# Optimization experiments

Measured on AMD Instinct MI355X. Metric: run time of the kernel, lower is better.

## Reference

```python
import jax, jax.numpy as jnp
import numpy as np
import math

D_MODEL = 512
NHEAD = 8
D_K = D_MODEL // NHEAD
WINDOW = 128
BATCH = 1
SEQ = 4096
NEG = -1e9  # matches torch masked_fill value


def setup_inputs() -> dict:
    key = jax.random.key(0)
    ks = jax.random.split(key, 9)
    s = 1.0 / math.sqrt(D_MODEL)
    return {
        "x": jax.random.normal(ks[0], (BATCH, SEQ, D_MODEL), dtype=jnp.float32),
        "wq": jax.random.uniform(ks[1], (D_MODEL, D_MODEL), jnp.float32, -s, s),
        "bq": jax.random.uniform(ks[2], (D_MODEL,), jnp.float32, -s, s),
        "wk": jax.random.uniform(ks[3], (D_MODEL, D_MODEL), jnp.float32, -s, s),
        "bk": jax.random.uniform(ks[4], (D_MODEL,), jnp.float32, -s, s),
        "wv": jax.random.uniform(ks[5], (D_MODEL, D_MODEL), jnp.float32, -s, s),
        "bv": jax.random.uniform(ks[6], (D_MODEL,), jnp.float32, -s, s),
        "wo": jax.random.uniform(ks[7], (D_MODEL, D_MODEL), jnp.float32, -s, s),
        "bo": jax.random.uniform(ks[8], (D_MODEL,), jnp.float32, -s, s),
    }


def reference(x, wq, bq, wk, bk, wv, bv, wo, bo):
    B, S, D = x.shape
    # projections -> (B, H, S, d_k)
    q = (x @ wq.T + bq).reshape(B, S, NHEAD, D_K).transpose(0, 2, 1, 3)
    k = (x @ wk.T + bk).reshape(B, S, NHEAD, D_K).transpose(0, 2, 1, 3)
    v = (x @ wv.T + bv).reshape(B, S, NHEAD, D_K).transpose(0, 2, 1, 3)
    # dense scores, band-masked (faithful to original: full S x S)
    scores = jnp.einsum('bhqd,bhkd->bhqk', q, k) / math.sqrt(D_K)
    idx = jnp.arange(S)
    band = jnp.abs(idx[:, None] - idx[None, :]) <= WINDOW  # (S, S)
    scores = jnp.where(band[None, None], scores, NEG)
    attn = jax.nn.softmax(scores, axis=-1)  # (B, H, S, S)
    ctx = jnp.einsum('bhqk,bhkd->bhqd', attn, v)
    ctx = ctx.transpose(0, 2, 1, 3).reshape(B, S, D)
    out = ctx @ wo.T + bo
    return out, attn
```

## Files before the change

kernel.cpp:

```cpp
#include <hip/hip_runtime.h>
#include <hip/hip_bf16.h>
#include <math.h>

#define S 4096
#define D 512
#define H 8
#define DK 64
#define WIN 128

typedef __attribute__((ext_vector_type(8))) short bf16x8;
typedef __attribute__((ext_vector_type(4))) float f32x4;

__device__ __forceinline__ unsigned short f2bf(float f) {
    __hip_bfloat16 h = __float2bfloat16(f);
    return *(unsigned short*)&h;
}

__global__ __launch_bounds__(256) void conv_bf16_kernel(
    const float* __restrict__ in, unsigned short* __restrict__ out, int n)
{
    const int i = (blockIdx.x * 256 + threadIdx.x) * 8;
    if (i >= n) return;
    float4 a = *(const float4*)&in[i];
    float4 b = *(const float4*)&in[i + 4];
    ushort4 o0 = {f2bf(a.x), f2bf(a.y), f2bf(a.z), f2bf(a.w)};
    ushort4 o1 = {f2bf(b.x), f2bf(b.y), f2bf(b.z), f2bf(b.w)};
    *(ushort4*)&out[i]     = o0;
    *(ushort4*)&out[i + 4] = o1;
}

__device__ __forceinline__ void mfma_gemm_body(
    const unsigned short* __restrict__ A,
    const float* __restrict__ W,
    const float* __restrict__ bias,
    float* __restrict__ C,
    unsigned short* __restrict__ CB)
{
    __shared__ unsigned short Bs[64][520];

    const int tid  = threadIdx.x;
    const int m0   = blockIdx.x * 128;
    const int n0   = blockIdx.y * 64;
    const int wv   = tid >> 6;
    const int lane = tid & 63;
    const int l16  = lane & 15;
    const int klo  = (lane >> 4) * 8;

    #pragma unroll
    for (int it = 0; it < 16; ++it) {
        const int c   = tid + it * 256;
        const int row = c >> 6;
        const int kc  = (c & 63) * 8;
        const float* src = &W[(size_t)(n0 + row) * 512 + kc];
        float4 a = *(const float4*)&src[0];
        float4 b = *(const float4*)&src[4];
        ushort4 o0 = {f2bf(a.x), f2bf(a.y), f2bf(a.z), f2bf(a.w)};
        ushort4 o1 = {f2bf(b.x), f2bf(b.y), f2bf(b.z), f2bf(b.w)};
        *(ushort4*)&Bs[row][kc]     = o0;
        *(ushort4*)&Bs[row][kc + 4] = o1;
    }
    __syncthreads();

    const unsigned short* arow0 = &A[(size_t)(m0 + wv * 32 + l16) * 512 + klo];
    const unsigned short* arow1 = arow0 + 16 * 512;

    f32x4 acc[2][4];
    #pragma unroll
    for (int r = 0; r < 2; ++r)
        #pragma unroll
        for (int nf = 0; nf < 4; ++nf)
            acc[r][nf] = (f32x4){0.f, 0.f, 0.f, 0.f};

    #pragma unroll 4
    for (int kb = 0; kb < 512; kb += 32) {
        bf16x8 a0 = *(const bf16x8*)&arow0[kb];
        bf16x8 a1 = *(const bf16x8*)&arow1[kb];
        #pragma unroll
        for (int nf = 0; nf < 4; ++nf) {
            bf16x8 b = *(const bf16x8*)&Bs[nf * 16 + l16][kb + klo];
            acc[0][nf] = __builtin_amdgcn_mfma_f32_16x16x32_bf16(a0, b, acc[0][nf], 0, 0, 0);
            acc[1][nf] = __builtin_amdgcn_mfma_f32_16x16x32_bf16(a1, b, acc[1][nf], 0, 0, 0);
        }
    }

    const int r0 = (lane >> 4) * 4;
    #pragma unroll
    for (int r = 0; r < 2; ++r) {
        #pragma unroll
        for (int nf = 0; nf < 4; ++nf) {
            const int col = n0 + nf * 16 + l16;
            const float bb = bias[col];
            #pragma unroll
            for (int vv = 0; vv < 4; ++vv) {
                const int row = m0 + wv * 32 + r * 16 + r0 + vv;
                const float val = acc[r][nf][vv] + bb;
                if (C)  C [(size_t)row * 512 + col] = val;
                if (CB) CB[(size_t)row * 512 + col] = f2bf(val);
            }
        }
    }
}

__global__ __launch_bounds__(256) void proj3_kernel(
    const unsigned short* __restrict__ xb,
    const float* __restrict__ wq, const float* __restrict__ bq,
    const float* __restrict__ wk, const float* __restrict__ bk,
    const float* __restrict__ wv, const float* __restrict__ bv,
    unsigned short* __restrict__ qb, unsigned short* __restrict__ kb,
    unsigned short* __restrict__ vb)
{
    const float* W; const float* b; unsigned short* CB;
    if (blockIdx.z == 0)      { W = wq; b = bq; CB = qb; }
    else if (blockIdx.z == 1) { W = wk; b = bk; CB = kb; }
    else                      { W = wv; b = bv; CB = vb; }
    mfma_gemm_body(xb, W, b, nullptr, CB);
}

__global__ __launch_bounds__(256) void outproj_kernel(
    const unsigned short* __restrict__ ctxb,
    const float* __restrict__ wo, const float* __restrict__ bo,
    float* __restrict__ out)
{
    mfma_gemm_body(ctxb, wo, bo, out, nullptr);
}

__global__ __launch_bounds__(256) void band_attn_kernel(
    const unsigned short* __restrict__ qb, const unsigned short* __restrict__ kb,
    const unsigned short* __restrict__ vb,
    float* __restrict__ attn, unsigned short* __restrict__ ctxb)
{
    __shared__ __align__(16) unsigned short Qs[16][72];
    __shared__ __align__(16) unsigned short KV[64][72];
    __shared__ float P[16][336];
    __shared__ float rinvs[16];

    const int tid = threadIdx.x;
    const int h  = blockIdx.y;
    const int q0 = blockIdx.x * 16;
    const int w0 = q0 - 128;

    const int wv   = tid >> 6;
    const int lane = tid & 63;
    const int l16  = lane & 15;
    const int klo  = (lane >> 4) * 8;
    const int r0   = (lane >> 4) * 4;

    {
        const int row = tid >> 4;
        const int db  = (tid & 15) * 4;
        *(ushort4*)&Qs[row][db] =
            *(const ushort4*)&qb[(size_t)(q0 + row) * 512 + h * 64 + db];
    }

    const int lr = tid >> 2;
    const int ld = (tid & 3) * 16;

    for (int ch = 0; ch < 5; ++ch) {
        const int c0 = w0 + ch * 64;
        if (c0 + 64 <= 0 || c0 >= S) continue;
        __syncthreads();
        {
            const int krow = min(max(c0 + lr, 0), S - 1);
            const unsigned short* src = &kb[(size_t)krow * 512 + h * 64 + ld];
            *(bf16x8*)&KV[lr][ld]     = *(const bf16x8*)&src[0];
            *(bf16x8*)&KV[lr][ld + 8] = *(const bf16x8*)&src[8];
        }
        __syncthreads();

        f32x4 acc = (f32x4){0.f, 0.f, 0.f, 0.f};
        #pragma unroll
        for (int kk = 0; kk < 64; kk += 32) {
            bf16x8 a = *(const bf16x8*)&Qs[l16][kk + klo];
            bf16x8 b = *(const bf16x8*)&KV[wv * 16 + l16][kk + klo];
            acc = __builtin_amdgcn_mfma_f32_16x16x32_bf16(a, b, acc, 0, 0, 0);
        }
        #pragma unroll
        for (int vv = 0; vv < 4; ++vv)
            P[r0 + vv][ch * 64 + wv * 16 + l16] = acc[vv] * 0.125f;
    }
    __syncthreads();

    {
        const int r   = tid >> 4;
        const int lx  = tid & 15;
        const int i   = q0 + r;
        const int lo = max(i - WIN, 0) - w0;
        const int hi = min(i + WIN, S - 1) - w0;

        float m = -1e30f;
        for (int c = lo + lx; c <= hi; c += 16) m = fmaxf(m, P[r][c]);
        m = fmaxf(m, __shfl_xor(m, 1));
        m = fmaxf(m, __shfl_xor(m, 2));
        m = fmaxf(m, __shfl_xor(m, 4));
        m = fmaxf(m, __shfl_xor(m, 8));

        float sum = 0.f;
        for (int c = lx; c < 320; c += 16) {
            float e = 0.f;
            if (c >= lo && c <= hi) {
                e = __expf(P[r][c] - m);
                sum += e;
            }
            P[r][c] = e;
        }
        sum += __shfl_xor(sum, 1);
        sum += __shfl_xor(sum, 2);
        sum += __shfl_xor(sum, 4);
        sum += __shfl_xor(sum, 8);
        if (lx == 0) rinvs[r] = 1.0f / sum;
    }

    f32x4 pacc = (f32x4){0.f, 0.f, 0.f, 0.f};
    for (int ch = 0; ch < 5; ++ch) {
        const int c0 = w0 + ch * 64;
        if (c0 + 64 <= 0 || c0 >= S) continue;
        __syncthreads();
        {
            const int vrow = min(max(c0 + lr, 0), S - 1);
            ushort4 v0 = *(const ushort4*)&vb[(size_t)vrow * 512 + h * 64 + ld];
            ushort4 v1 = *(const ushort4*)&vb[(size_t)vrow * 512 + h * 64 + ld + 4];
            ushort4 v2 = *(const ushort4*)&vb[(size_t)vrow * 512 + h * 64 + ld + 8];
            ushort4 v3 = *(const ushort4*)&vb[(size_t)vrow * 512 + h * 64 + ld + 12];
            KV[ld +  0][lr] = v0.x; KV[ld +  1][lr] = v0.y;
            KV[ld +  2][lr] = v0.z; KV[ld +  3][lr] = v0.w;
            KV[ld +  4][lr] = v1.x; KV[ld +  5][lr] = v1.y;
            KV[ld +  6][lr] = v1.z; KV[ld +  7][lr] = v1.w;
            KV[ld +  8][lr] = v2.x; KV[ld +  9][lr] = v2.y;
            KV[ld + 10][lr] = v2.z; KV[ld + 11][lr] = v2.w;
            KV[ld + 12][lr] = v3.x; KV[ld + 13][lr] = v3.y;
            KV[ld + 14][lr] = v3.z; KV[ld + 15][lr] = v3.w;
        }
        __syncthreads();

        #pragma unroll
        for (int kk = 0; kk < 64; kk += 32) {
            unsigned short abuf[8];
            #pragma unroll
            for (int e = 0; e < 8; ++e)
                abuf[e] = f2bf(P[l16][ch * 64 + kk + klo + e]);
            bf16x8 a = *(const bf16x8*)abuf;
            bf16x8 b = *(const bf16x8*)&KV[wv * 16 + l16][kk + klo];
            pacc = __builtin_amdgcn_mfma_f32_16x16x32_bf16(a, b, pacc, 0, 0, 0);
        }
    }

    #pragma unroll
    for (int vv = 0; vv < 4; ++vv) {
        const int row = q0 + r0 + vv;
        ctxb[(size_t)row * 512 + h * 64 + wv * 16 + l16] =
            f2bf(pacc[vv] * rinvs[r0 + vv]);
    }

    float* rowbase = attn + (size_t)h * S * S;
    #pragma unroll 1
    for (int r = 0; r < 16; ++r) {
        const int i = q0 + r;
        float* rowp = rowbase + (size_t)i * S;
        const int lo = max(i - WIN, 0) - w0;
        const int hi = min(i + WIN, S - 1) - w0;
        const float rv = rinvs[r];
        #pragma unroll
        for (int t = 0; t < 4; ++t) {
            const int c4 = (tid + t * 256) << 2;
            const int lc = c4 - w0;
            float4 o;
            if (lc >= lo && lc + 3 <= hi) {
                float4 p = *(const float4*)&P[r][lc];
                o.x = p.x * rv; o.y = p.y * rv; o.z = p.z * rv; o.w = p.w * rv;
            } else if (lc + 3 < lo || lc > hi) {
                o = make_float4(0.f, 0.f, 0.f, 0.f);
            } else {
                o.x = (lc + 0 >= lo && lc + 0 <= hi) ? P[r][lc + 0] * rv : 0.f;
                o.y = (lc + 1 >= lo && lc + 1 <= hi) ? P[r][lc + 1] * rv : 0.f;
                o.z = (lc + 2 >= lo && lc + 2 <= hi) ? P[r][lc + 2] * rv : 0.f;
                o.w = (lc + 3 >= lo && lc + 3 <= hi) ? P[r][lc + 3] * rv : 0.f;
            }
            *(float4*)&rowp[c4] = o;
        }
    }
}

extern "C" void kernel_launch(void* const* d_in, const int* in_sizes, int n_in,
                              void* d_out, int out_size, void* d_ws, size_t ws_size,
                              hipStream_t stream)
{
    (void)in_sizes; (void)n_in; (void)out_size; (void)ws_size;
    const float* x  = (const float*)d_in[0];
    const float* wq = (const float*)d_in[1];
    const float* bq = (const float*)d_in[2];
    const float* wk = (const float*)d_in[3];
    const float* bk = (const float*)d_in[4];
    const float* wv = (const float*)d_in[5];
    const float* bv = (const float*)d_in[6];
    const float* wo = (const float*)d_in[7];
    const float* bo = (const float*)d_in[8];

    float* out  = (float*)d_out;
    float* attn = out + (size_t)S * D;

    unsigned short* xb   = (unsigned short*)d_ws;
    unsigned short* qb   = xb   + (size_t)S * D;
    unsigned short* kb   = qb   + (size_t)S * D;
    unsigned short* vb   = kb   + (size_t)S * D;
    unsigned short* ctxb = vb   + (size_t)S * D;

    conv_bf16_kernel<<<(S * D) / (256 * 8), 256, 0, stream>>>(x, xb, S * D);
    proj3_kernel<<<dim3(32, 8, 3), 256, 0, stream>>>(xb, wq, bq, wk, bk, wv, bv, qb, kb, vb);
    band_attn_kernel<<<dim3(256, 8), 256, 0, stream>>>(qb, kb, vb, attn, ctxb);
    outproj_kernel<<<dim3(32, 8), 256, 0, stream>>>(ctxb, wo, bo, out);
}
```

Measured before the change: 153.3 us.

## Pre-convert weights to bf16, read B from global, warp-local KV staging, nontemporal attn stores

All weight matrices are converted to bf16 once in the conversion kernel, so the GEMM blocks no longer convert fp32 weights into shared memory and instead read bf16 B fragments straight from global memory. In the band attention kernel, each wave now stages only the K/V rows it consumes, and the block-wide barriers around each chunk are replaced by a local LDS wait. The large attn output is written with nontemporal stores to reduce cache pollution. The GEMM now relies on cache hits for B reuse rather than LDS, and the conversion kernel launches many idle blocks for the smaller weight tensors.

```diff
diff --git a/kernel.cpp b/kernel.cpp
--- a/kernel.cpp
+++ b/kernel.cpp
@@ -17,27 +17,38 @@
 }
 
 __global__ __launch_bounds__(256) void conv_bf16_kernel(
-    const float* __restrict__ in, unsigned short* __restrict__ out, int n)
-{
+    const float* __restrict__ x,
+    const float* __restrict__ wq, const float* __restrict__ wk,
+    const float* __restrict__ wv, const float* __restrict__ wo,
+    unsigned short* __restrict__ xb,
+    unsigned short* __restrict__ wqb, unsigned short* __restrict__ wkb,
+    unsigned short* __restrict__ wvb, unsigned short* __restrict__ wob)
+{
+    const float* src; unsigned short* dst; int n;
+    switch (blockIdx.y) {
+        case 0:  src = x;  dst = xb;  n = S * D; break;
+        case 1:  src = wq; dst = wqb; n = D * D; break;
+        case 2:  src = wk; dst = wkb; n = D * D; break;
+        case 3:  src = wv; dst = wvb; n = D * D; break;
+        default: src = wo; dst = wob; n = D * D; break;
+    }
     const int i = (blockIdx.x * 256 + threadIdx.x) * 8;
     if (i >= n) return;
-    float4 a = *(const float4*)&in[i];
-    float4 b = *(const float4*)&in[i + 4];
+    float4 a = *(const float4*)&src[i];
+    float4 b = *(const float4*)&src[i + 4];
     ushort4 o0 = {f2bf(a.x), f2bf(a.y), f2bf(a.z), f2bf(a.w)};
     ushort4 o1 = {f2bf(b.x), f2bf(b.y), f2bf(b.z), f2bf(b.w)};
-    *(ushort4*)&out[i]     = o0;
-    *(ushort4*)&out[i + 4] = o1;
+    *(ushort4*)&dst[i]     = o0;
+    *(ushort4*)&dst[i + 4] = o1;
 }
 
 __device__ __forceinline__ void mfma_gemm_body(
     const unsigned short* __restrict__ A,
-    const float* __restrict__ W,
+    const unsigned short* __restrict__ W16,
     const float* __restrict__ bias,
     float* __restrict__ C,
     unsigned short* __restrict__ CB)
 {
-    __shared__ unsigned short Bs[64][520];
-
     const int tid  = threadIdx.x;
     const int m0   = blockIdx.x * 128;
     const int n0   = blockIdx.y * 64;
@@ -46,23 +57,9 @@
     const int l16  = lane & 15;
     const int klo  = (lane >> 4) * 8;
 
-    #pragma unroll
-    for (int it = 0; it < 16; ++it) {
-        const int c   = tid + it * 256;
-        const int row = c >> 6;
-        const int kc  = (c & 63) * 8;
-        const float* src = &W[(size_t)(n0 + row) * 512 + kc];
-        float4 a = *(const float4*)&src[0];
-        float4 b = *(const float4*)&src[4];
-        ushort4 o0 = {f2bf(a.x), f2bf(a.y), f2bf(a.z), f2bf(a.w)};
-        ushort4 o1 = {f2bf(b.x), f2bf(b.y), f2bf(b.z), f2bf(b.w)};
-        *(ushort4*)&Bs[row][kc]     = o0;
-        *(ushort4*)&Bs[row][kc + 4] = o1;
-    }
-    __syncthreads();
-
     const unsigned short* arow0 = &A[(size_t)(m0 + wv * 32 + l16) * 512 + klo];
     const unsigned short* arow1 = arow0 + 16 * 512;
+    const unsigned short* brow  = &W16[(size_t)(n0 + l16) * 512 + klo];
 
     f32x4 acc[2][4];
     #pragma unroll
@@ -77,7 +74,7 @@
         bf16x8 a1 = *(const bf16x8*)&arow1[kb];
         #pragma unroll
         for (int nf = 0; nf < 4; ++nf) {
-            bf16x8 b = *(const bf16x8*)&Bs[nf * 16 + l16][kb + klo];
+            bf16x8 b = *(const bf16x8*)&brow[nf * 16 * 512 + kb];
             acc[0][nf] = __builtin_amdgcn_mfma_f32_16x16x32_bf16(a0, b, acc[0][nf], 0, 0, 0);
             acc[1][nf] = __builtin_amdgcn_mfma_f32_16x16x32_bf16(a1, b, acc[1][nf], 0, 0, 0);
         }
@@ -103,25 +100,25 @@
 
 __global__ __launch_bounds__(256) void proj3_kernel(
     const unsigned short* __restrict__ xb,
-    const float* __restrict__ wq, const float* __restrict__ bq,
-    const float* __restrict__ wk, const float* __restrict__ bk,
-    const float* __restrict__ wv, const float* __restrict__ bv,
+    const unsigned short* __restrict__ wqb, const float* __restrict__ bq,
+    const unsigned short* __restrict__ wkb, const float* __restrict__ bk,
+    const unsigned short* __restrict__ wvb, const float* __restrict__ bv,
     unsigned short* __restrict__ qb, unsigned short* __restrict__ kb,
     unsigned short* __restrict__ vb)
 {
-    const float* W; const float* b; unsigned short* CB;
-    if (blockIdx.z == 0)      { W = wq; b = bq; CB = qb; }
-    else if (blockIdx.z == 1) { W = wk; b = bk; CB = kb; }
-    else                      { W = wv; b = bv; CB = vb; }
+    const unsigned short* W; const float* b; unsigned short* CB;
+    if (blockIdx.z == 0)      { W = wqb; b = bq; CB = qb; }
+    else if (blockIdx.z == 1) { W = wkb; b = bk; CB = kb; }
+    else                      { W = wvb; b = bv; CB = vb; }
     mfma_gemm_body(xb, W, b, nullptr, CB);
 }
 
 __global__ __launch_bounds__(256) void outproj_kernel(
     const unsigned short* __restrict__ ctxb,
-    const float* __restrict__ wo, const float* __restrict__ bo,
+    const unsigned short* __restrict__ wob, const float* __restrict__ bo,
     float* __restrict__ out)
 {
-    mfma_gemm_body(ctxb, wo, bo, out, nullptr);
+    mfma_gemm_body(ctxb, wob, bo, out, nullptr);
 }
 
 __global__ __launch_bounds__(256) void band_attn_kernel(
@@ -151,21 +148,20 @@
         *(ushort4*)&Qs[row][db] =
             *(const ushort4*)&qb[(size_t)(q0 + row) * 512 + h * 64 + db];
     }
-
-    const int lr = tid >> 2;
-    const int ld = (tid & 3) * 16;
+    __syncthreads();
 
     for (int ch = 0; ch < 5; ++ch) {
         const int c0 = w0 + ch * 64;
         if (c0 + 64 <= 0 || c0 >= S) continue;
-        __syncthreads();
         {
-            const int krow = min(max(c0 + lr, 0), S - 1);
-            const unsigned short* src = &kb[(size_t)krow * 512 + h * 64 + ld];
-            *(bf16x8*)&KV[lr][ld]     = *(const bf16x8*)&src[0];
-            *(bf16x8*)&KV[lr][ld + 8] = *(const bf16x8*)&src[8];
-        }
-        __syncthreads();
+            const int kcol = wv * 16 + (lane & 15);
+            const int dd   = (lane >> 4) * 16;
+            const int krow = min(max(c0 + kcol, 0), S - 1);
+            const unsigned short* src = &kb[(size_t)krow * 512 + h * 64 + dd];
+            *(bf16x8*)&KV[kcol][dd]     = *(const bf16x8*)&src[0];
+            *(bf16x8*)&KV[kcol][dd + 8] = *(const bf16x8*)&src[8];
+        }
+        asm volatile("s_waitcnt lgkmcnt(0)" ::: "memory");
 
         f32x4 acc = (f32x4){0.f, 0.f, 0.f, 0.f};
         #pragma unroll
@@ -209,28 +205,30 @@
         sum += __shfl_xor(sum, 8);
         if (lx == 0) rinvs[r] = 1.0f / sum;
     }
+    __syncthreads();
 
     f32x4 pacc = (f32x4){0.f, 0.f, 0.f, 0.f};
     for (int ch = 0; ch < 5; ++ch) {
         const int c0 = w0 + ch * 64;
         if (c0 + 64 <= 0 || c0 >= S) continue;
-        __syncthreads();
         {
-            const int vrow = min(max(c0 + lr, 0), S - 1);
-            ushort4 v0 = *(const ushort4*)&vb[(size_t)vrow * 512 + h * 64 + ld];
-            ushort4 v1 = *(const ushort4*)&vb[(size_t)vrow * 512 + h * 64 + ld + 4];
-            ushort4 v2 = *(const ushort4*)&vb[(size_t)vrow * 512 + h * 64 + ld + 8];
-            ushort4 v3 = *(const ushort4*)&vb[(size_t)vrow * 512 + h * 64 + ld + 12];
-            KV[ld +  0][lr] = v0.x; KV[ld +  1][lr] = v0.y;
-            KV[ld +  2][lr] = v0.z; KV[ld +  3][lr] = v0.w;
-            KV[ld +  4][lr] = v1.x; KV[ld +  5][lr] = v1.y;
-            KV[ld +  6][lr] = v1.z; KV[ld +  7][lr] = v1.w;
-            KV[ld +  8][lr] = v2.x; KV[ld +  9][lr] = v2.y;
-            KV[ld + 10][lr] = v2.z; KV[ld + 11][lr] = v2.w;
-            KV[ld + 12][lr] = v3.x; KV[ld + 13][lr] = v3.y;
-            KV[ld + 14][lr] = v3.z; KV[ld + 15][lr] = v3.w;
-        }
-        __syncthreads();
+            const int col  = lane;
+            const int vrow = min(max(c0 + col, 0), S - 1);
+            const unsigned short* src = &vb[(size_t)vrow * 512 + h * 64 + wv * 16];
+            ushort4 v0 = *(const ushort4*)&src[0];
+            ushort4 v1 = *(const ushort4*)&src[4];
+            ushort4 v2 = *(const ushort4*)&src[8];
+            ushort4 v3 = *(const ushort4*)&src[12];
+            KV[wv * 16 +  0][col] = v0.x; KV[wv * 16 +  1][col] = v0.y;
+            KV[wv * 16 +  2][col] = v0.z; KV[wv * 16 +  3][col] = v0.w;
+            KV[wv * 16 +  4][col] = v1.x; KV[wv * 16 +  5][col] = v1.y;
+            KV[wv * 16 +  6][col] = v1.z; KV[wv * 16 +  7][col] = v1.w;
+            KV[wv * 16 +  8][col] = v2.x; KV[wv * 16 +  9][col] = v2.y;
+            KV[wv * 16 + 10][col] = v2.z; KV[wv * 16 + 11][col] = v2.w;
+            KV[wv * 16 + 12][col] = v3.x; KV[wv * 16 + 13][col] = v3.y;
+            KV[wv * 16 + 14][col] = v3.z; KV[wv * 16 + 15][col] = v3.w;
+        }
+        asm volatile("s_waitcnt lgkmcnt(0)" ::: "memory");
 
         #pragma unroll
         for (int kk = 0; kk < 64; kk += 32) {
@@ -263,19 +261,19 @@
         for (int t = 0; t < 4; ++t) {
             const int c4 = (tid + t * 256) << 2;
             const int lc = c4 - w0;
-            float4 o;
+            f32x4 o;
             if (lc >= lo && lc + 3 <= hi) {
-                float4 p = *(const float4*)&P[r][lc];
-                o.x = p.x * rv; o.y = p.y * rv; o.z = p.z * rv; o.w = p.w * rv;
+                f32x4 p = *(const f32x4*)&P[r][lc];
+                o = p * rv;
             } else if (lc + 3 < lo || lc > hi) {
-                o = make_float4(0.f, 0.f, 0.f, 0.f);
+                o = (f32x4){0.f, 0.f, 0.f, 0.f};
             } else {
-                o.x = (lc + 0 >= lo && lc + 0 <= hi) ? P[r][lc + 0] * rv : 0.f;
-                o.y = (lc + 1 >= lo && lc + 1 <= hi) ? P[r][lc + 1] * rv : 0.f;
-                o.z = (lc + 2 >= lo && lc + 2 <= hi) ? P[r][lc + 2] * rv : 0.f;
-                o.w = (lc + 3 >= lo && lc + 3 <= hi) ? P[r][lc + 3] * rv : 0.f;
+                o[0] = (lc + 0 >= lo && lc + 0 <= hi) ? P[r][lc + 0] * rv : 0.f;
+                o[1] = (lc + 1 >= lo && lc + 1 <= hi) ? P[r][lc + 1] * rv : 0.f;
+                o[2] = (lc + 2 >= lo && lc + 2 <= hi) ? P[r][lc + 2] * rv : 0.f;
+                o[3] = (lc + 3 >= lo && lc + 3 <= hi) ? P[r][lc + 3] * rv : 0.f;
             }
-            *(float4*)&rowp[c4] = o;
+            __builtin_nontemporal_store(o, (f32x4*)&rowp[c4]);
         }
     }
 }
@@ -303,9 +301,15 @@
     unsigned short* kb   = qb   + (size_t)S * D;
     unsigned short* vb   = kb   + (size_t)S * D;
     unsigned short* ctxb = vb   + (size_t)S * D;
-
-    conv_bf16_kernel<<<(S * D) / (256 * 8), 256, 0, stream>>>(x, xb, S * D);
-    proj3_kernel<<<dim3(32, 8, 3), 256, 0, stream>>>(xb, wq, bq, wk, bk, wv, bv, qb, kb, vb);
+    unsigned short* wqb  = ctxb + (size_t)S * D;
+    unsigned short* wkb  = wqb  + (size_t)D * D;
+    unsigned short* wvb  = wkb  + (size_t)D * D;
+    unsigned short* wob  = wvb  + (size_t)D * D;
+
+    conv_bf16_kernel<<<dim3(1024, 5), 256, 0, stream>>>(
+        x, wq, wk, wv, wo, xb, wqb, wkb, wvb, wob);
+    proj3_kernel<<<dim3(32, 8, 3), 256, 0, stream>>>(
+        xb, wqb, bq, wkb, bk, wvb, bv, qb, kb, vb);
     band_attn_kernel<<<dim3(256, 8), 256, 0, stream>>>(qb, kb, vb, attn, ctxb);
-    outproj_kernel<<<dim3(32, 8), 256, 0, stream>>>(ctxb, wo, bo, out);
-}
+    outproj_kernel<<<dim3(32, 8), 256, 0, stream>>>(ctxb, wob, bo, out);
+}
```

After: 174.1 us. +13.6%, slower.
